# Optimization experiments

Measured on AMD Instinct MI355X. Metric: run time of the kernel, lower is better.

Reference implementation:

```python
import jax, jax.numpy as jnp
import numpy as np

N = 100000      # nodes
E = 1600000     # edges (before self loops)
F_X = 30        # raw node feature dim
F_IN = 32       # pos(2) + x(30)
H = 64          # GAT hidden size
G = 64          # graphs in batch
MID = 32        # linear intermediate
C = 10          # num classes
NEG_SLOPE = 0.2 # PyG GATConv default leaky-relu slope


def setup_inputs() -> dict:
    key = jax.random.key(0)
    ks = jax.random.split(key, 16)
    inp = {}
    inp["x"] = jax.random.normal(ks[0], (N, F_X), jnp.float32)
    inp["pos"] = jax.random.normal(ks[1], (N, 2), jnp.float32)
    inp["edge_index"] = jax.random.randint(ks[2], (2, E), 0, N, dtype=jnp.int32)
    inp["batch"] = jnp.sort(jax.random.randint(ks[3], (N,), 0, G, dtype=jnp.int32))
    # GATConv params (heads=1): W [in,out], att_src/att_dst [out], bias [out]
    for i, (fi, fo) in enumerate([(F_IN, H), (H, H)]):
        sc = 1.0 / np.sqrt(fi)
        inp[f"gat{i}_W"] = jax.random.normal(ks[4 + 3 * i], (fi, fo), jnp.float32) * sc
        inp[f"gat{i}_att_src"] = jax.random.normal(ks[5 + 3 * i], (fo,), jnp.float32) * 0.1
        inp[f"gat{i}_att_dst"] = jax.random.normal(ks[6 + 3 * i], (fo,), jnp.float32) * 0.1
        inp[f"gat{i}_bias"] = jnp.zeros((fo,), jnp.float32)
    # Linear head params
    for i, (fi, fo) in enumerate([(H, MID), (MID, C)]):
        sc = 1.0 / np.sqrt(fi)
        inp[f"lin{i}_W"] = jax.random.normal(ks[10 + 2 * i], (fi, fo), jnp.float32) * sc
        inp[f"lin{i}_b"] = jnp.zeros((fo,), jnp.float32)
    return inp


def _gat_conv(h, src, dst, W, a_src, a_dst, b):
    """PyG GATConv, heads=1, with self loops already appended to src/dst.
    message j->i on edge (src=j, dst=i): alpha = softmax_i(leakyrelu(a_src.h'_j + a_dst.h'_i))."""
    n = h.shape[0]
    hp = h @ W                                         # [N, out]
    e = jax.nn.leaky_relu((hp @ a_src)[src] + (hp @ a_dst)[dst], NEG_SLOPE)  # [E']
    m = jax.lax.stop_gradient(jax.ops.segment_max(e, dst, num_segments=n))
    w = jnp.exp(e - m[dst])                            # [E']
    denom = jax.ops.segment_sum(w, dst, num_segments=n)  # [N]
    agg = jax.ops.segment_sum(hp[src] * w[:, None], dst, num_segments=n)  # [N, out]
    return agg / denom[:, None] + b


def reference(x, pos, gat0_W, gat0_att_src, gat0_att_dst, gat0_bias,
              gat1_W, gat1_att_src, gat1_att_dst, gat1_bias,
              lin0_W, lin0_b, lin1_W, lin1_b, edge_index, batch):
    n = x.shape[0]
    loop = jnp.arange(n, dtype=edge_index.dtype)
    src = jnp.concatenate([edge_index[0], loop])       # add self loops (PyG default)
    dst = jnp.concatenate([edge_index[1], loop])
    h = jnp.concatenate([pos, x], axis=1)              # [N, F_IN]
    h = _gat_conv(h, src, dst, gat0_W, gat0_att_src, gat0_att_dst, gat0_bias)
    h = _gat_conv(h, src, dst, gat1_W, gat1_att_src, gat1_att_dst, gat1_bias)
    # global mean pool over graphs
    cnt = jax.ops.segment_sum(jnp.ones((n,), h.dtype), batch, num_segments=G)
    g = jax.ops.segment_sum(h, batch, num_segments=G) / jnp.maximum(cnt, 1.0)[:, None]
    # dropout(p=0.2) is identity in eval mode
    g = jax.nn.relu(g @ lin0_W + lin0_b)
    g = jax.nn.relu(g @ lin1_W + lin1_b)
    return g
```

## Files before the change

kernel.cpp:

```cpp
#include <hip/hip_runtime.h>
#include <hip/hip_fp16.h>

#define NEG_SLOPE 0.2f

__device__ __forceinline__ float lrelu(float x) { return x > 0.f ? x : NEG_SLOPE * x; }
__device__ __forceinline__ float rdlane(float v, int k) {
    return __int_as_float(__builtin_amdgcn_readlane(__float_as_int(v), k));
}


__global__ void k_cnt(const int* __restrict__ dst, int E, int NB, int EB,
                      int* __restrict__ cnt) {
    __shared__ int h[400];
    int t = threadIdx.x, blk = blockIdx.x;
    for (int i = t; i < NB; i += 256) h[i] = 0;
    __syncthreads();
    int e0 = blk * 4096;
    for (int i = t; i < 4096; i += 256) {
        int e = e0 + i;
        if (e < E) atomicAdd(&h[dst[e] >> 8], 1);
    }
    __syncthreads();
    for (int i = t; i < NB; i += 256) cnt[(size_t)i * EB + blk] = h[i];
}

__global__ void k_btot(const int* __restrict__ cnt, int EB, int* __restrict__ tot) {
    __shared__ int sd[256];
    int b = blockIdx.x, t = threadIdx.x;
    int v = 0;
    for (int i = t; i < EB; i += 256) v += cnt[(size_t)b * EB + i];
    sd[t] = v;
    __syncthreads();
    for (int o = 128; o; o >>= 1) {
        if (t < o) sd[t] += sd[t + o];
        __syncthreads();
    }
    if (!t) tot[b] = sd[0];
}

__global__ void k_bscan(const int* __restrict__ tot, int NB, int E, int* __restrict__ bOff,
                        float* __restrict__ gpool, int GP) {
    __shared__ int sd[512];
    int t = threadIdx.x;
    for (int i = t; i < GP; i += 512) gpool[i] = 0.f;
    int v = (t < NB) ? tot[t] : 0;
    sd[t] = v;
    __syncthreads();
    for (int o = 1; o < 512; o <<= 1) {
        int a = (t >= o) ? sd[t - o] : 0;
        __syncthreads();
        sd[t] += a;
        __syncthreads();
    }
    if (t < NB) bOff[t] = sd[t] - v;
    if (t == 0) bOff[NB] = E;
}

__global__ void k_bbase(const int* __restrict__ cnt, const int* __restrict__ bOff, int EB,
                        int* __restrict__ base) {
    __shared__ int sd[512];
    int b = blockIdx.x, t = threadIdx.x;
    int v = (t < EB) ? cnt[(size_t)b * EB + t] : 0;
    sd[t] = v;
    __syncthreads();
    for (int o = 1; o < 512; o <<= 1) {
        int a = (t >= o) ? sd[t - o] : 0;
        __syncthreads();
        sd[t] += a;
        __syncthreads();
    }
    if (t < EB) base[b * EB + t] = bOff[b] + sd[t] - v;
}

__global__ void k_bin(const int* __restrict__ src, const int* __restrict__ dst, int E,
                      int NB, int EB, const int* __restrict__ base, int* __restrict__ pk) {
    __shared__ int cur[400];
    __shared__ int baseL[400];
    int t = threadIdx.x, blk = blockIdx.x;
    int e0 = blk * 4096;
    int ne = E - e0 < 4096 ? E - e0 : 4096;
    for (int i = t; i < NB; i += 256) {
        cur[i] = 0;
        baseL[i] = base[i * EB + blk];
    }
    __syncthreads();
    for (int i = t; i < ne; i += 256) {
        int d_ = dst[e0 + i], s_ = src[e0 + i];
        int bk = d_ >> 8;
        int r = atomicAdd(&cur[bk], 1);
        pk[baseL[bk] + r] = (s_ << 8) | (d_ & 255);
    }
}

__global__ void k_csr(const int* __restrict__ pk, const int* __restrict__ bOff, int N,
                      int E, int NB, int* __restrict__ offs, int* __restrict__ adj) {
    const int CAP = 4608;
    __shared__ int stage[4608];
    __shared__ int cnt[256];
    __shared__ int cur[256];
    int b = blockIdx.x;
    int t = threadIdx.x;
    int lo = b << 8;
    int e0 = bOff[b], e1 = bOff[b + 1];
    int ne = e1 - e0;
    cnt[t] = 0;
    __syncthreads();
    for (int i = t; i < ne; i += 256) {
        int v = pk[e0 + i];
        if (i < CAP) stage[i] = v;
        atomicAdd(&cnt[v & 255], 1);
    }
    __syncthreads();
    int v = cnt[t];
    __syncthreads();
    for (int off = 1; off < 256; off <<= 1) {
        int add = (t >= off) ? cnt[t - off] : 0;
        __syncthreads();
        cnt[t] += add;
        __syncthreads();
    }
    int excl = cnt[t] - v;
    cur[t] = excl;
    if (lo + t < N) offs[lo + t] = e0 + excl;
    if (b == 0 && t == 0) offs[N] = E;
    __syncthreads();
    for (int i = t; i < ne; i += 256) {
        int ed = (i < CAP) ? stage[i] : pk[e0 + i];
        int p = e0 + atomicAdd(&cur[ed & 255], 1);
        adj[p] = ed >> 8;
    }
}


__global__ void k_mm0(const float* __restrict__ pos, const float* __restrict__ x,
                      const float* __restrict__ W, const float* __restrict__ asrc,
                      const float* __restrict__ adst, int n, __half* __restrict__ hp,
                      float* __restrict__ s, float* __restrict__ d) {
    int lane = threadIdx.x & 63;
    int wv = threadIdx.x >> 6;
    int base = (blockIdx.x * 4 + wv) * 8;
    if (base >= n) return;
    float hm[8];
#pragma unroll
    for (int m = 0; m < 8; m++) {
        int nd = base + m < n ? base + m : n - 1;
        float v = 0.f;
        if (lane < 2) v = pos[(size_t)nd * 2 + lane];
        else if (lane < 32) v = x[(size_t)nd * 30 + lane - 2];
        hm[m] = v;
    }
    float acc[8] = {0.f, 0.f, 0.f, 0.f, 0.f, 0.f, 0.f, 0.f};
    for (int k = 0; k < 32; k++) {
        float wk = W[k * 64 + lane];
#pragma unroll
        for (int m = 0; m < 8; m++) acc[m] += rdlane(hm[m], k) * wk;
    }
    float as = asrc[lane], ad = adst[lane];
#pragma unroll
    for (int m = 0; m < 8; m++) {
        int nd = base + m;
        if (nd < n) hp[(size_t)nd * 64 + lane] = __float2half(acc[m]);
        float sv = acc[m] * as;
        float dv = acc[m] * ad;
#pragma unroll
        for (int off = 32; off; off >>= 1) {
            sv += __shfl_xor(sv, off);
            dv += __shfl_xor(dv, off);
        }
        if (lane == 0 && nd < n) {
            s[nd] = sv;
            d[nd] = dv;
        }
    }
}

__global__ void k_mm(const float* __restrict__ h, const float* __restrict__ W,
                     const float* __restrict__ asrc, const float* __restrict__ adst, int n,
                     __half* __restrict__ hp, float* __restrict__ s, float* __restrict__ d) {
    int lane = threadIdx.x & 63;
    int wv = threadIdx.x >> 6;
    int base = (blockIdx.x * 4 + wv) * 8;
    if (base >= n) return;
    float hm[8];
#pragma unroll
    for (int m = 0; m < 8; m++) {
        int nd = base + m < n ? base + m : n - 1;
        hm[m] = h[(size_t)nd * 64 + lane];
    }
    float acc[8] = {0.f, 0.f, 0.f, 0.f, 0.f, 0.f, 0.f, 0.f};
    for (int k = 0; k < 64; k++) {
        float wk = W[k * 64 + lane];
#pragma unroll
        for (int m = 0; m < 8; m++) acc[m] += rdlane(hm[m], k) * wk;
    }
    float as = asrc[lane], ad = adst[lane];
#pragma unroll
    for (int m = 0; m < 8; m++) {
        int nd = base + m;
        if (nd < n) hp[(size_t)nd * 64 + lane] = __float2half(acc[m]);
        float sv = acc[m] * as;
        float dv = acc[m] * ad;
#pragma unroll
        for (int off = 32; off; off >>= 1) {
            sv += __shfl_xor(sv, off);
            dv += __shfl_xor(dv, off);
        }
        if (lane == 0 && nd < n) {
            s[nd] = sv;
            d[nd] = dv;
        }
    }
}

__global__ void k_agg(const int* __restrict__ offs, const int* __restrict__ adj,
                      const __half* __restrict__ hp, const float* __restrict__ s,
                      const float* __restrict__ dd, const float* __restrict__ bias, int n,
                      float* __restrict__ out) {
    int lane = threadIdx.x & 63;
    int node = blockIdx.x * 4 + (threadIdx.x >> 6);
    if (node >= n) return;
    int qw = lane >> 4;
    int fl = lane & 15;
    const char* hpB = (const char*)hp;
    float di = dd[node];
    int e0 = offs[node], e1 = offs[node + 1];
    int total = e1 - e0 + 1;
    int totalU = __builtin_amdgcn_readfirstlane(total);

    float4 acc = make_float4(0.f, 0.f, 0.f, 0.f);
    float wsum;

    if (totalU <= 64) {
        bool valid = lane < totalU;
        int j = node;
        if (lane > 0 && valid) j = adj[e0 + lane - 1];
        float sv = valid ? s[j] : -INFINITY;
        float ev = lrelu(sv + di);
        float m = ev;
#pragma unroll
        for (int off = 32; off; off >>= 1) m = fmaxf(m, __shfl_xor(m, off));
        float wgt = valid ? expf(ev - m) : 0.f;
        float ws = wgt;
#pragma unroll
        for (int off = 32; off; off >>= 1) ws += __shfl_xor(ws, off);
        wsum = ws;
        int wbits = __float_as_int(wgt);
#pragma unroll 4
        for (int i = 0; i < totalU; i += 4) {
            int ib = (i + qw) << 2;
            int jj = __builtin_amdgcn_ds_bpermute(ib, j);
            float ww = __int_as_float(__builtin_amdgcn_ds_bpermute(ib, wbits));
            uint2 rv = *(const uint2*)(hpB + (((unsigned)jj << 7) | ((unsigned)fl << 3)));
            float2 f01 = __half22float2(*reinterpret_cast<__half2*>(&rv.x));
            float2 f23 = __half22float2(*reinterpret_cast<__half2*>(&rv.y));
            acc.x += f01.x * ww;
            acc.y += f01.y * ww;
            acc.z += f23.x * ww;
            acc.w += f23.y * ww;
        }
    } else {
        float m = -INFINITY;
        for (int base = 0; base < totalU; base += 64) {
            int idx = base + lane;
            bool valid = idx < totalU;
            int j = node;
            if (idx > 0 && valid) j = adj[e0 + idx - 1];
            float sv = valid ? s[j] : -INFINITY;
            m = fmaxf(m, lrelu(sv + di));
        }
#pragma unroll
        for (int off = 32; off; off >>= 1) m = fmaxf(m, __shfl_xor(m, off));
        float ws = 0.f;
        for (int base = 0; base < totalU; base += 64) {
            int idx = base + lane;
            bool valid = idx < totalU;
            int j = node;
            if (idx > 0 && valid) j = adj[e0 + idx - 1];
            float sv = valid ? s[j] : -INFINITY;
            float wgt = valid ? expf(lrelu(sv + di) - m) : 0.f;
            ws += wgt;
            int cU = totalU - base < 64 ? totalU - base : 64;
            int wbits = __float_as_int(wgt);
#pragma unroll 4
            for (int i = 0; i < cU; i += 4) {
                int ib = (i + qw) << 2;
                int jj = __builtin_amdgcn_ds_bpermute(ib, j);
                float ww = __int_as_float(__builtin_amdgcn_ds_bpermute(ib, wbits));
                uint2 rv =
                    *(const uint2*)(hpB + (((unsigned)jj << 7) | ((unsigned)fl << 3)));
                float2 f01 = __half22float2(*reinterpret_cast<__half2*>(&rv.x));
                float2 f23 = __half22float2(*reinterpret_cast<__half2*>(&rv.y));
                acc.x += f01.x * ww;
                acc.y += f01.y * ww;
                acc.z += f23.x * ww;
                acc.w += f23.y * ww;
            }
        }
#pragma unroll
        for (int off = 32; off; off >>= 1) ws += __shfl_xor(ws, off);
        wsum = ws;
    }
#pragma unroll
    for (int off = 32; off >= 16; off >>= 1) {
        acc.x += __shfl_xor(acc.x, off);
        acc.y += __shfl_xor(acc.y, off);
        acc.z += __shfl_xor(acc.z, off);
        acc.w += __shfl_xor(acc.w, off);
    }
    if (qw == 0) {
        float inv = 1.0f / wsum;
        float4 b4 = ((const float4*)bias)[fl];
        float4 o;
        o.x = acc.x * inv + b4.x;
        o.y = acc.y * inv + b4.y;
        o.z = acc.z * inv + b4.z;
        o.w = acc.w * inv + b4.w;
        ((float4*)out)[(size_t)node * 16 + fl] = o;
    }
}

__global__ void k_pool1(const float* __restrict__ h, const int* __restrict__ batch, int n,
                        float* __restrict__ pool) {
    int lane = threadIdx.x & 63;
    int wv = threadIdx.x >> 6;
    int base = blockIdx.x * 256 + wv * 64;
    if (base >= n) return;
    int cnt = n - base < 64 ? n - base : 64;
    int g0 = batch[base];
    int g1 = batch[base + cnt - 1];
    if (g0 == g1 && cnt == 64) {
        float acc = 0.f;
#pragma unroll 8
        for (int k = 0; k < 64; k++) acc += h[(size_t)(base + k) * 64 + lane];
        atomicAdd(&pool[g0 * 64 + lane], acc);
        return;
    }
    int bl = batch[base + (lane < cnt ? lane : cnt - 1)];
    int cur = g0;
    float acc = 0.f;
    for (int k = 0; k < cnt; k++) {
        int g = __builtin_amdgcn_readlane(bl, k);
        if (g != cur) {
            atomicAdd(&pool[cur * 64 + lane], acc);
            acc = 0.f;
            cur = g;
        }
        acc += h[(size_t)(base + k) * 64 + lane];
    }
    atomicAdd(&pool[cur * 64 + lane], acc);
}

__global__ void k_head(const float* __restrict__ pool, const int* __restrict__ batch, int n,
                       const float* __restrict__ W0, const float* __restrict__ b0,
                       const float* __restrict__ W1, const float* __restrict__ b1,
                       float* __restrict__ out) {
    __shared__ float gs[64];
    __shared__ float mid[32];
    int i = blockIdx.x;
    int t = threadIdx.x;
    int lo = 0, hi = n;
    while (lo < hi) {
        int md = (lo + hi) >> 1;
        if (batch[md] < i) lo = md + 1; else hi = md;
    }
    int start = lo;
    lo = 0; hi = n;
    while (lo < hi) {
        int md = (lo + hi) >> 1;
        if (batch[md] < i + 1) lo = md + 1; else hi = md;
    }
    float cnt = (float)(lo - start);
    gs[t] = pool[i * 64 + t] / fmaxf(cnt, 1.f);
    __syncthreads();
    if (t < 32) {
        float a = b0[t];
#pragma unroll
        for (int k = 0; k < 64; k++) a += gs[k] * W0[k * 32 + t];
        mid[t] = fmaxf(a, 0.f);
    }
    __syncthreads();
    if (t < 10) {
        float a = b1[t];
#pragma unroll
        for (int k = 0; k < 32; k++) a += mid[k] * W1[k * 10 + t];
        out[i * 10 + t] = fmaxf(a, 0.f);
    }
}


extern "C" void kernel_launch(void* const* d_in, const int* in_sizes, int n_in,
                              void* d_out, int out_size, void* d_ws, size_t ws_size,
                              hipStream_t stream) {
    const float* x    = (const float*)d_in[0];
    const float* pos  = (const float*)d_in[1];
    const int*   ei   = (const int*)d_in[2];
    const int*   batch= (const int*)d_in[3];
    const float* g0W  = (const float*)d_in[4];
    const float* g0as = (const float*)d_in[5];
    const float* g0ad = (const float*)d_in[6];
    const float* g0b  = (const float*)d_in[7];
    const float* g1W  = (const float*)d_in[8];
    const float* g1as = (const float*)d_in[9];
    const float* g1ad = (const float*)d_in[10];
    const float* g1b  = (const float*)d_in[11];
    const float* l0W  = (const float*)d_in[12];
    const float* l0b  = (const float*)d_in[13];
    const float* l1W  = (const float*)d_in[14];
    const float* l1b  = (const float*)d_in[15];
    float* out = (float*)d_out;

    const int N = in_sizes[3];
    const int E = in_sizes[2] / 2;
    const int G = out_size / 10;
    const int NB = (N + 255) >> 8;
    const int EB = (E + 4095) / 4096;

    char* w = (char*)d_ws;
    auto alloc = [&](size_t bytes) {
        void* p = (void*)w;
        w += (bytes + 255) & ~(size_t)255;
        return p;
    };
    int* tot     = (int*)alloc((size_t)NB * 4);
    int* bOff    = (int*)alloc((size_t)(NB + 1) * 4);
    int* offs    = (int*)alloc((size_t)(N + 1) * 4);
    int* adj     = (int*)alloc((size_t)E * 4);
    __half* hp   = (__half*)alloc((size_t)N * 64 * 2);
    float* hbuf  = (float*)alloc((size_t)N * 64 * 4);
    float* sarr  = (float*)alloc((size_t)N * 4);
    float* darr  = (float*)alloc((size_t)N * 4);
    float* gpool = (float*)alloc((size_t)G * 64 * 4);
    int* pk   = (int*)hp;
    int* cnt  = (int*)hbuf;
    int* base = (int*)hbuf + (size_t)NB * EB;

    const int* esrc = ei;
    const int* edst = ei + E;

    k_cnt<<<EB, 256, 0, stream>>>(edst, E, NB, EB, cnt);
    k_btot<<<NB, 256, 0, stream>>>(cnt, EB, tot);
    k_bscan<<<1, 512, 0, stream>>>(tot, NB, E, bOff, gpool, G * 64);
    k_bbase<<<NB, 512, 0, stream>>>(cnt, bOff, EB, base);
    k_bin<<<EB, 256, 0, stream>>>(esrc, edst, E, NB, EB, base, pk);
    k_csr<<<NB, 256, 0, stream>>>(pk, bOff, N, E, NB, offs, adj);

    int aggBlocks = (N + 3) / 4;
    int mmBlocks = (N + 31) / 32;
    k_mm0<<<mmBlocks, 256, 0, stream>>>(pos, x, g0W, g0as, g0ad, N, hp, sarr, darr);
    k_agg<<<aggBlocks, 256, 0, stream>>>(offs, adj, hp, sarr, darr, g0b, N, hbuf);
    k_mm<<<mmBlocks, 256, 0, stream>>>(hbuf, g1W, g1as, g1ad, N, hp, sarr, darr);
    k_agg<<<aggBlocks, 256, 0, stream>>>(offs, adj, hp, sarr, darr, g1b, N, hbuf);
    k_pool1<<<NB, 256, 0, stream>>>(hbuf, batch, N, gpool);
    k_head<<<G, 64, 0, stream>>>(gpool, batch, N, l0W, l0b, l1W, l1b, out);
}
```

Measured before the change: 346.5 us.

## Process two nodes per wavefront in GAT aggregation and drop max-subtraction

The aggregation kernel now gives each node a half-wavefront of 32 lanes, so one 64-lane wave handles two nodes. Average degree is about 17, which left most lanes idle in the one-node-per-wave layout. The softmax max pass is also removed: weights use exp(e) directly instead of exp(e - max), which drops a reduction and, for high-degree nodes, a second pass over the adjacency. This risks overflow if attention logits grow large, and the loop trip count follows the larger degree of the two paired nodes.

```diff
diff --git a/kernel.cpp b/kernel.cpp
--- a/kernel.cpp
+++ b/kernel.cpp
@@ -217,37 +217,37 @@
                       const float* __restrict__ dd, const float* __restrict__ bias, int n,
                       float* __restrict__ out) {
     int lane = threadIdx.x & 63;
-    int node = blockIdx.x * 4 + (threadIdx.x >> 6);
-    if (node >= n) return;
-    int qw = lane >> 4;
+    int wv = threadIdx.x >> 6;
+    int half = lane >> 5;
+    int hl = lane & 31;
+    int node = blockIdx.x * 8 + wv * 2 + half;
+    bool nvalid = node < n;
+    int nd = nvalid ? node : n - 1;
+    const char* hpB = (const char*)hp;
+    float di = dd[nd];
+    int e0 = offs[nd], e1 = offs[nd + 1];
+    int total = e1 - e0 + 1;
+    int tm = max(total, __shfl_xor(total, 32));
+    int tU = __builtin_amdgcn_readfirstlane(tm);
+
     int fl = lane & 15;
-    const char* hpB = (const char*)hp;
-    float di = dd[node];
-    int e0 = offs[node], e1 = offs[node + 1];
-    int total = e1 - e0 + 1;
-    int totalU = __builtin_amdgcn_readfirstlane(total);
-
+    int sb = (lane & 32) + ((lane >> 4) & 1);
     float4 acc = make_float4(0.f, 0.f, 0.f, 0.f);
-    float wsum;
-
-    if (totalU <= 64) {
-        bool valid = lane < totalU;
-        int j = node;
-        if (lane > 0 && valid) j = adj[e0 + lane - 1];
-        float sv = valid ? s[j] : -INFINITY;
-        float ev = lrelu(sv + di);
-        float m = ev;
-#pragma unroll
-        for (int off = 32; off; off >>= 1) m = fmaxf(m, __shfl_xor(m, off));
-        float wgt = valid ? expf(ev - m) : 0.f;
-        float ws = wgt;
-#pragma unroll
-        for (int off = 32; off; off >>= 1) ws += __shfl_xor(ws, off);
-        wsum = ws;
-        int wbits = __float_as_int(wgt);
+    float ws = 0.f;
+
+    if (tU <= 32) {
+        bool valid = hl < total;
+        int j = nd;
+        if (hl > 0 && valid) j = adj[e0 + hl - 1];
+        float ev = lrelu((valid ? s[j] : 0.f) + di);
+        float w = valid ? expf(ev) : 0.f;
+        ws = w;
+#pragma unroll
+        for (int off = 16; off; off >>= 1) ws += __shfl_xor(ws, off);
+        int wbits = __float_as_int(w);
 #pragma unroll 4
-        for (int i = 0; i < totalU; i += 4) {
-            int ib = (i + qw) << 2;
+        for (int i = 0; 2 * i < tU; i++) {
+            int ib = (sb + 2 * i) << 2;
             int jj = __builtin_amdgcn_ds_bpermute(ib, j);
             float ww = __int_as_float(__builtin_amdgcn_ds_bpermute(ib, wbits));
             uint2 rv = *(const uint2*)(hpB + (((unsigned)jj << 7) | ((unsigned)fl << 3)));
@@ -259,31 +259,18 @@
             acc.w += f23.y * ww;
         }
     } else {
-        float m = -INFINITY;
-        for (int base = 0; base < totalU; base += 64) {
-            int idx = base + lane;
-            bool valid = idx < totalU;
-            int j = node;
+        for (int cb = 0; cb < tU; cb += 32) {
+            int idx = cb + hl;
+            bool valid = idx < total;
+            int j = nd;
             if (idx > 0 && valid) j = adj[e0 + idx - 1];
-            float sv = valid ? s[j] : -INFINITY;
-            m = fmaxf(m, lrelu(sv + di));
-        }
-#pragma unroll
-        for (int off = 32; off; off >>= 1) m = fmaxf(m, __shfl_xor(m, off));
-        float ws = 0.f;
-        for (int base = 0; base < totalU; base += 64) {
-            int idx = base + lane;
-            bool valid = idx < totalU;
-            int j = node;
-            if (idx > 0 && valid) j = adj[e0 + idx - 1];
-            float sv = valid ? s[j] : -INFINITY;
-            float wgt = valid ? expf(lrelu(sv + di) - m) : 0.f;
-            ws += wgt;
-            int cU = totalU - base < 64 ? totalU - base : 64;
-            int wbits = __float_as_int(wgt);
-#pragma unroll 4
-            for (int i = 0; i < cU; i += 4) {
-                int ib = (i + qw) << 2;
+            float ev = lrelu((valid ? s[j] : 0.f) + di);
+            float w = valid ? expf(ev) : 0.f;
+            ws += w;
+            int wbits = __float_as_int(w);
+            int cnt = tU - cb < 32 ? tU - cb : 32;
+            for (int i = 0; 2 * i < cnt; i++) {
+                int ib = (sb + 2 * i) << 2;
                 int jj = __builtin_amdgcn_ds_bpermute(ib, j);
                 float ww = __int_as_float(__builtin_amdgcn_ds_bpermute(ib, wbits));
                 uint2 rv =
@@ -297,18 +284,14 @@
             }
         }
 #pragma unroll
-        for (int off = 32; off; off >>= 1) ws += __shfl_xor(ws, off);
-        wsum = ws;
-    }
-#pragma unroll
-    for (int off = 32; off >= 16; off >>= 1) {
-        acc.x += __shfl_xor(acc.x, off);
-        acc.y += __shfl_xor(acc.y, off);
-        acc.z += __shfl_xor(acc.z, off);
-        acc.w += __shfl_xor(acc.w, off);
-    }
-    if (qw == 0) {
-        float inv = 1.0f / wsum;
+        for (int off = 16; off; off >>= 1) ws += __shfl_xor(ws, off);
+    }
+    acc.x += __shfl_xor(acc.x, 16);
+    acc.y += __shfl_xor(acc.y, 16);
+    acc.z += __shfl_xor(acc.z, 16);
+    acc.w += __shfl_xor(acc.w, 16);
+    if (!(lane & 16) && nvalid) {
+        float inv = 1.0f / ws;
         float4 b4 = ((const float4*)bias)[fl];
         float4 o;
         o.x = acc.x * inv + b4.x;
@@ -444,7 +427,7 @@
     k_bin<<<EB, 256, 0, stream>>>(esrc, edst, E, NB, EB, base, pk);
     k_csr<<<NB, 256, 0, stream>>>(pk, bOff, N, E, NB, offs, adj);
 
-    int aggBlocks = (N + 3) / 4;
+    int aggBlocks = (N + 7) / 8;
     int mmBlocks = (N + 31) / 32;
     k_mm0<<<mmBlocks, 256, 0, stream>>>(pos, x, g0W, g0as, g0ad, N, hp, sarr, darr);
     k_agg<<<aggBlocks, 256, 0, stream>>>(offs, adj, hp, sarr, darr, g0b, N, hbuf);
```

New measurement: 323.3 us. 6.7% less time.
